# Kernel tuning notes

Hardware: AMD Instinct MI355X
Metric: run time of the kernel (lower is better)

Reference implementation:

```python
import jax, jax.numpy as jnp
import numpy as np

NUM_GRAPHS = 10  # seq_len graphs batched together


def _gat_layer(x, W, al, ar, b, src, dst, n_nodes):
    # x: [N, h_dim]; W: [h_dim, H*D]; al/ar/b: [H, D]
    H, D = al.shape
    feat = (x @ W).reshape(-1, H, D)                      # [N, H, D]
    el = jnp.einsum('nhd,hd->nh', feat, al)               # [N, H]
    er = jnp.einsum('nhd,hd->nh', feat, ar)               # [N, H]
    e = jax.nn.leaky_relu(el[src] + er[dst], 0.2)         # [E, H]
    # edge softmax over incoming edges of each dst node (stable)
    emax = jax.ops.segment_max(e, dst, num_segments=n_nodes)
    emax = jnp.where(jnp.isfinite(emax), emax, 0.0)
    w = jnp.exp(e - emax[dst])                            # [E, H]
    denom = jax.ops.segment_sum(w, dst, num_segments=n_nodes)  # [N, H]
    msg = w[:, :, None] * feat[src]                       # [E, H, D]
    agg = jax.ops.segment_sum(msg, dst, num_segments=n_nodes)  # [N, H, D]
    out = agg / jnp.maximum(denom, 1e-9)[:, :, None] + b
    return out.mean(axis=1)                               # [N, h_dim] (mean over heads)


def setup_inputs() -> dict:
    key = jax.random.key(0)
    ks = jax.random.split(key, 16)
    N, E, V, h, H = 100000, 1000000, 50000, 64, 3
    node_ids = jax.random.randint(ks[0], (N,), 0, V)
    edge_src = jax.random.randint(ks[1], (E,), 0, N)
    edge_dst = jax.random.randint(ks[2], (E,), 0, N)
    node_graph_id = jnp.sort(jax.random.randint(ks[3], (N,), 0, NUM_GRAPHS))
    s = 1.0 / np.sqrt(h)
    return {
        'node_ids': node_ids, 'edge_src': edge_src, 'edge_dst': edge_dst,
        'node_graph_id': node_graph_id,
        'W_embed': jax.random.normal(ks[4], (V, h), jnp.float32),
        'W1': jax.random.normal(ks[5], (h, H * h), jnp.float32) * s,
        'al1': jax.random.normal(ks[6], (H, h), jnp.float32) * s,
        'ar1': jax.random.normal(ks[7], (H, h), jnp.float32) * s,
        'b1': jnp.zeros((H, h), jnp.float32),
        'W2': jax.random.normal(ks[8], (h, H * h), jnp.float32) * s,
        'al2': jax.random.normal(ks[9], (H, h), jnp.float32) * s,
        'ar2': jax.random.normal(ks[10], (H, h), jnp.float32) * s,
        'b2': jnp.zeros((H, h), jnp.float32),
    }


def reference(node_ids, edge_src, edge_dst, node_graph_id, W_embed,
              W1, al1, ar1, b1, W2, al2, ar2, b2):
    n_nodes = node_ids.shape[0]
    h = W_embed[node_ids]                                 # gather embeddings
    h = _gat_layer(h, W1, al1, ar1, b1, edge_src, edge_dst, n_nodes)
    h = _gat_layer(h, W2, al2, ar2, b2, edge_src, edge_dst, n_nodes)
    # dgl.max_nodes: per-graph max pooling over nodes
    global_info = jax.ops.segment_max(h, node_graph_id, num_segments=NUM_GRAPHS)
    return global_info                                    # [NUM_GRAPHS, h_dim]
```

## Files before the change

### kernel.cpp

```cpp
#include <hip/hip_runtime.h>
#include <math.h>


#define HEADS 3
#define HD 64
#define FDIM (HEADS*HD)
#define NCOL 208
#define NUM_GRAPHS 10
#define NPB 32
#define FROWB 384
#define PREPB 104

typedef short bf16x8 __attribute__((ext_vector_type(8)));
typedef float f32x4  __attribute__((ext_vector_type(4)));

__device__ __forceinline__ float bf2f(unsigned short u) {
    return __uint_as_float(((unsigned int)u) << 16);
}
__device__ __forceinline__ unsigned short f2bf(float f) {
    unsigned int u = __float_as_uint(f);
    unsigned int r = (u + 0x7FFFu + ((u >> 16) & 1u)) >> 16;
    return (unsigned short)r;
}

__device__ __forceinline__ int wave_incl_scan(int v, int lane) {
#pragma unroll
    for (int off = 1; off < 64; off <<= 1) {
        int t = __shfl_up(v, off);
        if (lane >= off) v += t;
    }
    return v;
}

__device__ __forceinline__ unsigned int fmap(float f) {
    unsigned int u = __float_as_uint(f);
    return (u & 0x80000000u) ? ~u : (u | 0x80000000u);
}
__device__ __forceinline__ float funmap(unsigned int u) {
    u = (u & 0x80000000u) ? (u & 0x7FFFFFFFu) : ~u;
    return __uint_as_float(u);
}

__global__ void k_prep_hist(const float* __restrict__ W1, const float* __restrict__ al1,
                            const float* __restrict__ ar1,
                            const float* __restrict__ W2, const float* __restrict__ al2,
                            const float* __restrict__ ar2,
                            unsigned short* __restrict__ Wt1, unsigned short* __restrict__ Wt2,
                            unsigned int* __restrict__ gm,
                            const int* __restrict__ dst, int* __restrict__ deg, int E) {
    if (blockIdx.x < PREPB) {
        int i = blockIdx.x * blockDim.x + threadIdx.x;
        if (i < 2 * NCOL * HD) {
            int l = i / (NCOL * HD), j = i % (NCOL * HD);
            int c = j >> 6, k = j & 63;
            const float* W  = l ? W2  : W1;
            const float* al = l ? al2 : al1;
            const float* ar = l ? ar2 : ar1;
            unsigned short* Wt = l ? Wt2 : Wt1;
            float v = 0.f;
            if (c < FDIM) {
                v = W[k * FDIM + c];
            } else if (c < FDIM + 6) {
                int h = c - FDIM;
                const float* a = (h < 3) ? al : ar;
                int hh = (h < 3) ? h : h - 3;
                float s = 0.f;
                for (int d = 0; d < HD; ++d)
                    s += W[k * FDIM + hh * HD + d] * a[hh * HD + d];
                v = s;
            }
            Wt[j] = f2bf(v);
        }
        if (i < NUM_GRAPHS * HD) gm[i] = 0x007FFFFFu;
    } else {
        int i = (blockIdx.x - PREPB) * blockDim.x + threadIdx.x;
        if (i < E) atomicAdd(&deg[dst[i]], 1);
    }
}

__global__ void k_scan1(const int* __restrict__ deg, int* __restrict__ tmp,
                        int* __restrict__ partials, int N) {
    int t = threadIdx.x, b = blockIdx.x;
    int i = b * 256 + t;
    int v = (i < N) ? deg[i] : 0;
    int lane = t & 63, w = t >> 6;
    int incl = wave_incl_scan(v, lane);
    __shared__ int wsum[4];
    if (lane == 63) wsum[w] = incl;
    __syncthreads();
    int off = 0;
    for (int j = 0; j < w; ++j) off += wsum[j];
    incl += off;
    if (i < N) tmp[i] = incl;
    if (t == 255) partials[b] = incl;
}

__global__ void k_scan2(int* __restrict__ partials, int nb) {
    int t = threadIdx.x;
    int v = (t < nb) ? partials[t] : 0;
    int lane = t & 63, w = t >> 6;
    int incl = wave_incl_scan(v, lane);
    __shared__ int wsum[8];
    if (lane == 63) wsum[w] = incl;
    __syncthreads();
    int off = 0;
    for (int j = 0; j < w; ++j) off += wsum[j];
    incl += off;
    if (t < nb) partials[t] = incl;
}

__global__ void k_scan3(const int* __restrict__ tmp, const int* __restrict__ deg,
                        const int* __restrict__ partials, int* __restrict__ rowptr,
                        int* __restrict__ cur, int N) {
    int i = blockIdx.x * blockDim.x + threadIdx.x;
    if (i >= N) return;
    int b = i >> 8;
    int off = b ? partials[b - 1] : 0;
    int incl = tmp[i] + off;
    rowptr[i + 1] = incl;
    cur[i] = incl - deg[i];
    if (i == 0) rowptr[0] = 0;
}

__device__ __forceinline__ void feat_body(
        const unsigned short* __restrict__ xbf, const int* __restrict__ ids,
        const float* __restrict__ Wemb, const unsigned short* __restrict__ Wt,
        unsigned char* __restrict__ featB, float4* __restrict__ el4,
        float4* __restrict__ er4, int N, int blk) {
    __shared__ unsigned short xs[NPB][72];
    __shared__ unsigned short ls[NPB][200];
    int t = threadIdx.x;
    int lane = t & 63, w = t >> 6;
    int base = blk * NPB;

    if (ids) {
        for (int i = t; i < NPB * 16; i += 256) {
            int row = i >> 4, c4 = (i & 15) * 4;
            int n = base + row;
            float4 v = {0.f, 0.f, 0.f, 0.f};
            if (n < N) v = *(const float4*)(Wemb + (size_t)ids[n] * HD + c4);
            unsigned short* dp = &xs[row][c4];
            dp[0] = f2bf(v.x); dp[1] = f2bf(v.y); dp[2] = f2bf(v.z); dp[3] = f2bf(v.w);
        }
    } else {
        for (int i = t; i < NPB * 16; i += 256) {
            int row = i >> 4, c4 = (i & 15) * 4;
            int n = base + row;
            ushort4 v = {0, 0, 0, 0};
            if (n < N) v = *(const ushort4*)(xbf + (size_t)n * HD + c4);
            *(ushort4*)(&xs[row][c4]) = v;
        }
    }

    int ntile = (w == 3) ? 4 : 3;
    bf16x8 bfrag[4][2];
#pragma unroll
    for (int c = 0; c < 4; ++c) {
        if (c >= ntile) break;
#pragma unroll
        for (int kk = 0; kk < 2; ++kk) {
            int coln = (w * 3 + c) * 16 + (lane & 15);
            int k0 = kk * 32 + (lane >> 4) * 8;
            bfrag[c][kk] = *(const bf16x8*)(Wt + (size_t)coln * HD + k0);
        }
    }
    __syncthreads();

    f32x4 acc[2][4];
#pragma unroll
    for (int r = 0; r < 2; ++r)
#pragma unroll
        for (int c = 0; c < 4; ++c) acc[r][c] = (f32x4){0.f, 0.f, 0.f, 0.f};
#pragma unroll
    for (int r = 0; r < 2; ++r)
#pragma unroll
        for (int kk = 0; kk < 2; ++kk) {
            int row = r * 16 + (lane & 15);
            int k0 = kk * 32 + (lane >> 4) * 8;
            bf16x8 a = *(const bf16x8*)(&xs[row][k0]);
#pragma unroll
            for (int c = 0; c < 4; ++c) {
                if (c >= ntile) break;
                acc[r][c] = __builtin_amdgcn_mfma_f32_16x16x32_bf16(a, bfrag[c][kk], acc[r][c], 0, 0, 0);
            }
        }

#pragma unroll
    for (int r = 0; r < 2; ++r)
#pragma unroll
        for (int c = 0; c < 3; ++c) {
            int col = (w * 3 + c) * 16 + (lane & 15);
#pragma unroll
            for (int j = 0; j < 4; ++j) {
                int row = r * 16 + (lane >> 4) * 4 + j;
                ls[row][col] = f2bf(acc[r][c][j]);
            }
        }

    if (w == 3) {
        int col = lane & 15;
        if (col < 6) {
#pragma unroll
            for (int r = 0; r < 2; ++r)
#pragma unroll
                for (int j = 0; j < 4; ++j) {
                    int row = r * 16 + (lane >> 4) * 4 + j;
                    int n = base + row;
                    if (n < N) {
                        float v = acc[r][3][j];
                        if (col < 3) ((float*)&el4[n])[col] = v;
                        else         ((float*)&er4[n])[col - 3] = v;
                    }
                }
        }
    }
    __syncthreads();

    for (int i = t; i < NPB * 64; i += 256) {
        int row = i >> 6, d = i & 63;
        int n = base + row;
        if (n < N) {
            unsigned int u = ((unsigned int)ls[row][64 + d] << 16) | (unsigned int)ls[row][d];
            *(unsigned int*)(featB + (size_t)n * FROWB + d * 4) = u;
        }
    }
    for (int i = t; i < NPB * 32; i += 256) {
        int row = i >> 5, dd = (i & 31) * 2;
        int n = base + row;
        if (n < N) {
            unsigned int u = (unsigned int)ls[row][128 + dd] |
                             ((unsigned int)ls[row][128 + dd + 1] << 16);
            *(unsigned int*)(featB + (size_t)n * FROWB + 256 + dd * 2) = u;
        }
    }
}

__global__ __launch_bounds__(256) void k_feat_mfma(
        const unsigned short* __restrict__ xbf, const int* __restrict__ ids,
        const float* __restrict__ Wemb, const unsigned short* __restrict__ Wt,
        unsigned char* __restrict__ featB, float4* __restrict__ el4,
        float4* __restrict__ er4, int N) {
    feat_body(xbf, ids, Wemb, Wt, featB, el4, er4, N, blockIdx.x);
}

__global__ __launch_bounds__(256) void k_feat1_scatter(
        const int* __restrict__ ids, const float* __restrict__ Wemb,
        const unsigned short* __restrict__ Wt,
        unsigned char* __restrict__ featB, float4* __restrict__ el4,
        float4* __restrict__ er4, int N,
        const int* __restrict__ src, const int* __restrict__ dst,
        int* __restrict__ cur, int* __restrict__ csrc, int E) {
    int g = blockIdx.x / 9, r = blockIdx.x % 9;
    if (r < 4) {
        int fb = g * 4 + r;
        if (fb * NPB < N)
            feat_body(nullptr, ids, Wemb, Wt, featB, el4, er4, N, fb);
    } else {
        int sb = g * 5 + (r - 4);
        int i = sb * 256 + (int)threadIdx.x;
        if (i < E) {
            int pos = atomicAdd(&cur[dst[i]], 1);
            csrc[pos] = src[i];
        }
    }
}

__global__ void k_gather(const int* __restrict__ rowptr, const int* __restrict__ csrc,
                         const float4* __restrict__ el4, const float4* __restrict__ er4,
                         const unsigned char* __restrict__ featB,
                         const float* __restrict__ b,
                         unsigned short* __restrict__ xout, int N) {
    __shared__ float4 stage[4][64];
    int wid = (blockIdx.x * blockDim.x + threadIdx.x) >> 6;
    int lane = threadIdx.x & 63, w = (threadIdx.x >> 6) & 3;
    if (wid >= N) return;
    int beg = rowptr[wid], end = rowptr[wid + 1];
    int deg = end - beg;
    float4 er = er4[wid];
    float acc0 = 0.f, acc1 = 0.f, acc2 = 0.f;
    float ds0 = 0.f, ds1 = 0.f, ds2 = 0.f;
    for (int cb = 0; cb < deg; cb += 64) {
        int nch = min(64, deg - cb);
        if (lane < nch) {
            int s = csrc[beg + cb + lane];
            float4 l = el4[s];
            float e0 = l.x + er.x; e0 = e0 >= 0.f ? e0 : 0.2f * e0;
            float e1 = l.y + er.y; e1 = e1 >= 0.f ? e1 : 0.2f * e1;
            float e2 = l.z + er.z; e2 = e2 >= 0.f ? e2 : 0.2f * e2;
            float4 o;
            o.x = __int_as_float(s);
            o.y = __expf(e0); o.z = __expf(e1); o.w = __expf(e2);
            stage[w][lane] = o;
        }
        __builtin_amdgcn_wave_barrier();
#pragma unroll 4
        for (int j = 0; j < nch; ++j) {
            float4 e = stage[w][j];
            int s = __float_as_int(e.x);
            const unsigned char* frow = featB + (size_t)s * FROWB;
            unsigned int u01 = *(const unsigned int*)(frow + (size_t)lane * 4);
            unsigned short h2 = *(const unsigned short*)(frow + 256 + (size_t)lane * 2);
            float f0 = __uint_as_float(u01 << 16);
            float f1 = __uint_as_float(u01 & 0xffff0000u);
            acc0 = fmaf(e.y, f0, acc0);
            acc1 = fmaf(e.z, f1, acc1);
            acc2 = fmaf(e.w, bf2f(h2), acc2);
            ds0 += e.y; ds1 += e.z; ds2 += e.w;
        }
        __builtin_amdgcn_wave_barrier();
    }
    float o = (acc0 / fmaxf(ds0, 1e-9f) + b[lane])
            + (acc1 / fmaxf(ds1, 1e-9f) + b[HD + lane])
            + (acc2 / fmaxf(ds2, 1e-9f) + b[2 * HD + lane]);
    xout[(size_t)wid * HD + lane] = f2bf(o * (1.f / 3.f));
}

__global__ void k_gmax(const unsigned short* __restrict__ x, const int* __restrict__ gid,
                       unsigned int* __restrict__ gm, int N) {
    int lane = threadIdx.x;
    int base = blockIdx.x * 64;
    int endn = min(base + 64, N);
    int cur = -1;
    float m = 0.f;
    for (int n = base; n < endn; ++n) {
        int g = gid[n];
        float v = bf2f(x[(size_t)n * HD + lane]);
        if (g != cur) {
            if (cur >= 0) atomicMax(&gm[cur * HD + lane], fmap(m));
            cur = g; m = v;
        } else {
            m = fmaxf(m, v);
        }
    }
    if (cur >= 0) atomicMax(&gm[cur * HD + lane], fmap(m));
}

__global__ void k_gmax_final(const unsigned int* __restrict__ gm, float* __restrict__ out) {
    int i = blockIdx.x * blockDim.x + threadIdx.x;
    if (i < NUM_GRAPHS * HD) out[i] = funmap(gm[i]);
}

extern "C" void kernel_launch(void* const* d_in, const int* in_sizes, int n_in,
                              void* d_out, int out_size, void* d_ws, size_t ws_size,
                              hipStream_t stream) {
    const int*   node_ids = (const int*)d_in[0];
    const int*   edge_src = (const int*)d_in[1];
    const int*   edge_dst = (const int*)d_in[2];
    const int*   gid      = (const int*)d_in[3];
    const float* Wemb     = (const float*)d_in[4];
    const float* W1  = (const float*)d_in[5];
    const float* al1 = (const float*)d_in[6];
    const float* ar1 = (const float*)d_in[7];
    const float* b1  = (const float*)d_in[8];
    const float* W2  = (const float*)d_in[9];
    const float* al2 = (const float*)d_in[10];
    const float* ar2 = (const float*)d_in[11];
    const float* b2  = (const float*)d_in[12];

    int N = in_sizes[0];
    int E = in_sizes[1];

    char* p = (char*)d_ws;
    auto alloc = [&](size_t bytes) {
        char* r = p;
        p += (bytes + 255) & ~(size_t)255;
        return (void*)r;
    };
    int*   deg      = (int*)alloc((size_t)N * 4);
    int*   tmp      = (int*)alloc((size_t)N * 4);
    int*   partials = (int*)alloc(512 * 4);
    int*   rowptr   = (int*)alloc((size_t)(N + 1) * 4);
    int*   cur      = (int*)alloc((size_t)N * 4);
    int*   csrc     = (int*)alloc((size_t)E * 4);
    unsigned char* featB = (unsigned char*)alloc((size_t)N * FROWB);
    unsigned short* Wt1  = (unsigned short*)alloc((size_t)NCOL * HD * 2);
    unsigned short* Wt2  = (unsigned short*)alloc((size_t)NCOL * HD * 2);
    float4* el4     = (float4*)alloc((size_t)N * 16);
    float4* er4     = (float4*)alloc((size_t)N * 16);
    unsigned short* x1b = (unsigned short*)alloc((size_t)N * HD * 2);
    unsigned int* gm = (unsigned int*)alloc(NUM_GRAPHS * HD * 4);
    (void)ws_size;

    int nb = (N + 255) / 256;

    hipMemsetAsync(deg, 0, (size_t)N * 4, stream);
    k_prep_hist<<<dim3(PREPB + (E + 255) / 256), dim3(256), 0, stream>>>(
        W1, al1, ar1, W2, al2, ar2, Wt1, Wt2, gm, edge_dst, deg, E);
    k_scan1<<<dim3(nb), dim3(256), 0, stream>>>(deg, tmp, partials, N);
    k_scan2<<<dim3(1), dim3(512), 0, stream>>>(partials, nb);
    k_scan3<<<dim3(nb), dim3(256), 0, stream>>>(tmp, deg, partials, rowptr, cur, N);

    dim3 featGrid((N + NPB - 1) / NPB), featBlk(256);
    dim3 aggGrid((N * 64 + 255) / 256), aggBlk(256);

    int nf = (N + NPB - 1) / NPB;
    int ns = (E + 255) / 256;
    int ngroups = ((nf + 3) / 4 > (ns + 4) / 5) ? (nf + 3) / 4 : (ns + 4) / 5;
    dim3 fusedGrid(ngroups * 9);

    k_feat1_scatter<<<fusedGrid, featBlk, 0, stream>>>(
        node_ids, Wemb, Wt1, featB, el4, er4, N,
        edge_src, edge_dst, cur, csrc, E);
    k_gather<<<aggGrid, aggBlk, 0, stream>>>(rowptr, csrc, el4, er4, featB, b1, x1b, N);

    k_feat_mfma<<<featGrid, featBlk, 0, stream>>>(x1b, nullptr, nullptr, Wt2,
                                                  featB, el4, er4, N);
    k_gather<<<aggGrid, aggBlk, 0, stream>>>(rowptr, csrc, el4, er4, featB, b2, x1b, N);

    k_gmax<<<dim3((N + 63) / 64), dim3(64), 0, stream>>>(x1b, gid, gm, N);
    k_gmax_final<<<dim3(1), dim3(NUM_GRAPHS * HD), 0, stream>>>(gm, (float*)d_out);
}
```

Baseline: 297.5 us.

## Partition CSR scatter by destination range to localize atomics and writes

```diff
diff --git a/kernel.cpp b/kernel.cpp
--- a/kernel.cpp
+++ b/kernel.cpp
@@ -10,6 +10,7 @@
 #define NPB 32
 #define FROWB 384
 #define PREPB 104
+#define ECHUNK 1024
 
 typedef short bf16x8 __attribute__((ext_vector_type(8)));
 typedef float f32x4  __attribute__((ext_vector_type(4)));
@@ -249,19 +250,28 @@
         unsigned char* __restrict__ featB, float4* __restrict__ el4,
         float4* __restrict__ er4, int N,
         const int* __restrict__ src, const int* __restrict__ dst,
-        int* __restrict__ cur, int* __restrict__ csrc, int E) {
-    int g = blockIdx.x / 9, r = blockIdx.x % 9;
-    if (r < 4) {
-        int fb = g * 4 + r;
+        int* __restrict__ cur, int* __restrict__ csrc, int E,
+        int NS8, int nsc8) {
+    if ((int)blockIdx.x < nsc8) {
+        int s = blockIdx.x;
+        int lo = (s & 7) * NS8;
+        int hi = lo + NS8;
+        int i0 = (s >> 3) * ECHUNK + (int)threadIdx.x;
+#pragma unroll
+        for (int j = 0; j < ECHUNK / 256; ++j) {
+            int i = i0 + j * 256;
+            if (i < E) {
+                int d = dst[i];
+                if (d >= lo && d < hi) {
+                    int pos = atomicAdd(&cur[d], 1);
+                    csrc[pos] = src[i];
+                }
+            }
+        }
+    } else {
+        int fb = blockIdx.x - nsc8;
         if (fb * NPB < N)
             feat_body(nullptr, ids, Wemb, Wt, featB, el4, er4, N, fb);
-    } else {
-        int sb = g * 5 + (r - 4);
-        int i = sb * 256 + (int)threadIdx.x;
-        if (i < E) {
-            int pos = atomicAdd(&cur[dst[i]], 1);
-            csrc[pos] = src[i];
-        }
     }
 }
 
@@ -394,13 +404,14 @@
     dim3 aggGrid((N * 64 + 255) / 256), aggBlk(256);
 
     int nf = (N + NPB - 1) / NPB;
-    int ns = (E + 255) / 256;
-    int ngroups = ((nf + 3) / 4 > (ns + 4) / 5) ? (nf + 3) / 4 : (ns + 4) / 5;
-    dim3 fusedGrid(ngroups * 9);
+    int nchunks = (E + ECHUNK - 1) / ECHUNK;
+    int nsc8 = nchunks * 8;
+    int NS8 = (N + 7) / 8;
+    dim3 fusedGrid(nsc8 + nf);
 
     k_feat1_scatter<<<fusedGrid, featBlk, 0, stream>>>(
         node_ids, Wemb, Wt1, featB, el4, er4, N,
-        edge_src, edge_dst, cur, csrc, E);
+        edge_src, edge_dst, cur, csrc, E, NS8, nsc8);
     k_gather<<<aggGrid, aggBlk, 0, stream>>>(rowptr, csrc, el4, er4, featB, b1, x1b, N);
 
     k_feat_mfma<<<featGrid, featBlk, 0, stream>>>(x1b, nullptr, nullptr, Wt2,
```

Result: no change. 294.2 us (-1.1%).
